# Performance work log

Hardware: AMD Instinct MI355X
Metric: run time of the kernel (lower is better)

The kernel has to match this reference:

```python
import jax, jax.numpy as jnp
import numpy as np

VOCAB_FACTORS = (16, 16, 16, 8)   # prod = 32768 = vocab_size
DIM_FACTORS = (4, 4, 4, 4)        # prod = 256   = projection_dim
RANKS = (1, 16, 16, 16, 1)        # tt_rank = 16
NUM_CORES = 4


def _core_shapes():
    return [(RANKS[k], VOCAB_FACTORS[k], DIM_FACTORS[k], RANKS[k + 1])
            for k in range(NUM_CORES)]


def _vocab_strides():
    # big-endian mixed-radix decomposition of a flat vocab index
    strides = []
    s = 1
    for n in reversed(VOCAB_FACTORS):
        strides.append(s)
        s *= n
    return tuple(reversed(strides))


def tt_lookup(cores, idx):
    """Reconstruct embedding rows from TT cores.
    cores[k]: [r_k, n_k, m_k, r_{k+1}];  idx: int array [...].
    Returns [..., prod(m_k)]."""
    flat = idx.reshape(-1)                                # [Bf]
    res = jnp.ones((flat.shape[0], 1, 1), dtype=cores[0].dtype)  # [Bf, M=1, r=1]
    for core, n, st in zip(cores, VOCAB_FACTORS, _vocab_strides()):
        digit = (flat // st) % n                          # [Bf]
        g = jnp.moveaxis(core[:, digit], 1, 0)            # [Bf, r, m, r']
        res = jnp.einsum('bMr,brms->bMms', res, g)        # [Bf, M, m, r']
        res = res.reshape(res.shape[0], -1, res.shape[-1])  # [Bf, M*m, r']
    D = res.shape[1]
    return res[..., 0].reshape(idx.shape + (D,))


def setup_inputs() -> dict:
    key = jax.random.key(0)
    ks = jax.random.split(key, 12)
    B, NEG, V = 8192, 20, int(np.prod(VOCAB_FACTORS))
    inp = {
        'center_words': jax.random.randint(ks[0], (B, 1), 0, V),
        'target_words': jax.random.randint(ks[1], (B, 1), 0, V),
        'negative_words': jax.random.randint(ks[2], (B, NEG), 0, V),
    }
    # embedding_v: glorot-style init spread over cores
    for k, shp in enumerate(_core_shapes()):
        glorot_std = float(np.sqrt(2.0 / (shp[0] * shp[1] + shp[2] * shp[3])))
        inp[f'v_core{k}'] = glorot_std * jax.random.normal(ks[3 + k], shp, dtype=jnp.float32)
    # embedding_u: stddev=1e-4 per the module
    for k, shp in enumerate(_core_shapes()):
        inp[f'u_core{k}'] = 1e-4 * jax.random.normal(ks[7 + k], shp, dtype=jnp.float32)
    return inp


def reference(center_words, target_words, negative_words,
              v_core0, v_core1, v_core2, v_core3,
              u_core0, u_core1, u_core2, u_core3):
    v_cores = (v_core0, v_core1, v_core2, v_core3)
    u_cores = (u_core0, u_core1, u_core2, u_core3)
    center_embeds = tt_lookup(v_cores, center_words)      # [B, 1, D]
    target_embeds = tt_lookup(u_cores, target_words)      # [B, 1, D]
    neg_embeds = -tt_lookup(u_cores, negative_words)      # [B, K, D]
    # target.bmm(center^T).squeeze(2) -> [B, 1]
    positive_score = jnp.einsum('bsd,btd->bs', target_embeds, center_embeds)
    # sum over negatives then view [B, 1]
    negative_score = jnp.sum(
        jnp.einsum('bkd,btd->bk', neg_embeds, center_embeds),
        axis=1, keepdims=True)                            # [B, 1]
    loss = jax.nn.log_sigmoid(positive_score) + jax.nn.log_sigmoid(negative_score)
    return -jnp.mean(loss)
```

## Files before the change

### kernel.cpp

```cpp
#include <hip/hip_runtime.h>
#include <hip/hip_bf16.h>

#define DEVINL __device__ __forceinline__

constexpr int NNEG   = 20;
constexpr int NBATCH = 8192;
constexpr int NMAIN_BLOCKS = NBATCH / 4;

constexpr int OFF_H01V = 68608;
constexpr int OFF_H23V = 134144;
constexpr int OFF_H01U = 166912;
constexpr int OFF_H23U = 232448;
constexpr int OFF_PART = 265216;
constexpr int OFF_UTAB_F = 267268;
constexpr size_t UTAB4_BYTES = (size_t)32768 * 128;
constexpr size_t USCALE_BYTE_OFF = (size_t)OFF_UTAB_F * 4 + UTAB4_BYTES;
constexpr size_t WS_NEED_BYTES = USCALE_BYTE_OFF + (size_t)32768 * 4;

DEVINL float bfbits_to_f32(unsigned short h) {
  unsigned int u = ((unsigned int)h) << 16;
  float f;
  __builtin_memcpy(&f, &u, sizeof(f));
  return f;
}

DEVINL unsigned short f32_to_bfbits(float f) {
  __hip_bfloat16 h = __float2bfloat16(f);
  unsigned short hb;
  __builtin_memcpy(&hb, &h, 2);
  return hb;
}

DEVINL float ldconv(const void* s, int i, bool isF32) {
  return isF32 ? ((const float*)s)[i]
               : bfbits_to_f32(((const unsigned short*)s)[i]);
}

DEVINL bool sniff_is_f32(const void* probe) {
  const unsigned short* p = (const unsigned short*)probe;
  int insane = 0;
#pragma unroll 1
  for (int i = 0; i < 64; ++i) {
    unsigned short h = p[i];
    int e = (h >> 7) & 0xFF;
    if (h != 0 && (e < 90 || e > 140)) insane++;
  }
  return insane > 8;
}

__global__ __launch_bounds__(256) void tt_htables(
    const void* v0, const void* v1, const void* v2, const void* v3,
    const void* u0, const void* u1, const void* u2, const void* u3,
    float* __restrict__ ws) {
  __shared__ bool sIsF32;
  if (threadIdx.x == 0) sIsF32 = sniff_is_f32(v1);
  __syncthreads();
  const bool isF32 = sIsF32;

  int t = blockIdx.x * 256 + threadIdx.x;
  bool isU = t >= 98304;
  int lt = isU ? t - 98304 : t;
  const void* c0 = isU ? u0 : v0;
  const void* c1 = isU ? u1 : v1;
  const void* c2 = isU ? u2 : v2;
  const void* c3 = isU ? u3 : v3;
  float* dst = ws + (isU ? OFF_H01U : OFF_H01V);

  if (lt < 65536) {
    int combo = lt >> 8, e = lt & 255;
    int d0 = combo >> 4, d1 = combo & 15;
    int M01 = e >> 4, r2 = e & 15;
    int m0 = M01 >> 2, m1 = M01 & 3;
    float s = 0.f;
#pragma unroll
    for (int r1 = 0; r1 < 16; ++r1)
      s = fmaf(ldconv(c0, (d0 * 4 + m0) * 16 + r1, isF32),
               ldconv(c1, ((r1 * 16 + d1) * 4 + m1) * 16 + r2, isF32), s);
    dst[lt] = s;
  } else {
    int lt2 = lt - 65536;
    int combo = lt2 >> 8, e = lt2 & 255;
    int d2 = combo >> 3, d3 = combo & 7;
    int m23 = e >> 4, r2 = e & 15;
    int m2 = m23 >> 2, m3 = m23 & 3;
    float s = 0.f;
#pragma unroll
    for (int r3 = 0; r3 < 16; ++r3)
      s = fmaf(ldconv(c2, ((r2 * 16 + d2) * 4 + m2) * 16 + r3, isF32),
               ldconv(c3, (r3 * 8 + d3) * 4 + m3, isF32), s);
    dst[65536 + lt2] = s;
  }
}

DEVINL float4 ld4(const float* p) { return *reinterpret_cast<const float4*>(p); }

DEVINL float logsigf(float x) {
  return fminf(x, 0.0f) - log1pf(expf(-fabsf(x)));
}

__global__ __launch_bounds__(256) void tt_utab4(const float* __restrict__ ws,
                                                unsigned short* __restrict__ utab4,
                                                float* __restrict__ uscale) {
  const int w    = blockIdx.x * 4 + (threadIdx.x >> 6);
  const int l    = threadIdx.x & 63;
  const int lo   = w & 127;
  const int hi0  = (w >> 7) * 8;

  const float* Bt = ws + OFF_H23U + lo * 256 + (l & 3) * 64;
  float b[64];
#pragma unroll
  for (int i = 0; i < 16; ++i) *reinterpret_cast<float4*>(&b[4 * i]) = ld4(Bt + 4 * i);

  const float* Abase = ws + OFF_H01U + (size_t)hi0 * 256 + (l >> 2) * 16;

#pragma unroll
  for (int rr = 0; rr < 8; rr += 2) {
    float a0[16], a1[16];
#pragma unroll
    for (int i = 0; i < 4; ++i) {
      *reinterpret_cast<float4*>(&a0[4 * i]) = ld4(Abase + rr * 256 + 4 * i);
      *reinterpret_cast<float4*>(&a1[4 * i]) = ld4(Abase + (rr + 1) * 256 + 4 * i);
    }
    float e0[4] = {0.f, 0.f, 0.f, 0.f}, e1[4] = {0.f, 0.f, 0.f, 0.f};
#pragma unroll
    for (int r = 0; r < 16; ++r) {
#pragma unroll
      for (int j = 0; j < 4; ++j) {
        e0[j] = fmaf(a0[r], b[j * 16 + r], e0[j]);
        e1[j] = fmaf(a1[r], b[j * 16 + r], e1[j]);
      }
    }
    float m0 = fmaxf(fmaxf(fabsf(e0[0]), fabsf(e0[1])), fmaxf(fabsf(e0[2]), fabsf(e0[3])));
    float m1 = fmaxf(fmaxf(fabsf(e1[0]), fabsf(e1[1])), fmaxf(fabsf(e1[2]), fabsf(e1[3])));
#pragma unroll
    for (int off = 32; off > 0; off >>= 1) {
      m0 = fmaxf(m0, __shfl_xor(m0, off, 64));
      m1 = fmaxf(m1, __shfl_xor(m1, off, 64));
    }
    const float inv0 = (m0 > 0.f) ? 7.f / m0 : 0.f;
    const float inv1 = (m1 > 0.f) ? 7.f / m1 : 0.f;
    unsigned int p0 = 0, p1 = 0;
#pragma unroll
    for (int j = 0; j < 4; ++j) {
      p0 |= ((unsigned int)(__float2int_rn(e0[j] * inv0) & 15)) << (4 * j);
      p1 |= ((unsigned int)(__float2int_rn(e1[j] * inv1) & 15)) << (4 * j);
    }
    const size_t v0i = (size_t)(hi0 + rr) * 128 + lo;
    const size_t v1i = v0i + 128;
    utab4[v0i * 64 + l] = (unsigned short)p0;
    utab4[v1i * 64 + l] = (unsigned short)p1;
    if (l == 0) {
      uscale[v0i] = m0 * (1.f / 7.f);
      uscale[v1i] = m1 * (1.f / 7.f);
    }
  }
}

__global__ __launch_bounds__(256) void tt_main6(
    const int* __restrict__ cw, const int* __restrict__ tw, const int* __restrict__ nw,
    const float* __restrict__ ws, const unsigned short* __restrict__ utab4,
    const float* __restrict__ uscale, float* __restrict__ partials) {
  const int lane = threadIdx.x & 63;
  const int wid  = threadIdx.x >> 6;
  const int b    = blockIdx.x * 4 + wid;

  const int ci = cw[b];
  const int ti = tw[b];
  const int myneg = nw[b * NNEG + (lane < NNEG ? lane : 0)];

  float c[4] = {0.f, 0.f, 0.f, 0.f};
  {
    const float* A  = ws + OFF_H01V + (ci >> 7) * 256 + (lane >> 2) * 16;
    const float* Bt = ws + OFF_H23V + (ci & 127) * 256 + (lane & 3) * 64;
    float a[16];
#pragma unroll
    for (int i = 0; i < 4; ++i) *reinterpret_cast<float4*>(&a[4 * i]) = ld4(A + 4 * i);
#pragma unroll
    for (int j = 0; j < 4; ++j) {
#pragma unroll
      for (int i = 0; i < 4; ++i) {
        float4 bv = ld4(Bt + j * 16 + 4 * i);
        c[j] = fmaf(a[4 * i], bv.x,
               fmaf(a[4 * i + 1], bv.y,
               fmaf(a[4 * i + 2], bv.z,
               fmaf(a[4 * i + 3], bv.w, c[j]))));
      }
    }
  }

  float pos = 0.f, nacc = 0.f;
#pragma unroll
  for (int k = 0; k < 21; ++k) {
    int idx = (k == 0) ? ti : __shfl(myneg, k - 1, 64);
    idx = __builtin_amdgcn_readfirstlane(idx);
    const unsigned int u = utab4[(size_t)idx * 64 + lane];
    const float sc = uscale[idx];
    const float f0 = (float)(((int)((u)       & 15) ^ 8) - 8);
    const float f1 = (float)(((int)((u >> 4)  & 15) ^ 8) - 8);
    const float f2 = (float)(((int)((u >> 8)  & 15) ^ 8) - 8);
    const float f3 = (float)(((int)((u >> 12) & 15) ^ 8) - 8);
    float p = fmaf(f0, c[0], fmaf(f1, c[1], fmaf(f2, c[2], f3 * c[3]))) * sc;
    if (k == 0) pos = p; else nacc += p;
  }

#pragma unroll
  for (int off = 32; off > 0; off >>= 1) {
    pos  += __shfl_xor(pos, off, 64);
    nacc += __shfl_xor(nacc, off, 64);
  }

  __shared__ float sred[4];
  if (lane == 0) sred[wid] = -(logsigf(pos) + logsigf(-nacc));
  __syncthreads();
  if (threadIdx.x == 0)
    partials[blockIdx.x] = sred[0] + sred[1] + sred[2] + sred[3];
}

DEVINL void frag16(const float* __restrict__ A, const float* __restrict__ Bt,
                   int l, float e[4]) {
  const float* Ar = A + (l >> 2) * 16;
  const float* Br = Bt + (l & 3) * 64;
  float a[16], bb[64];
#pragma unroll
  for (int i = 0; i < 4; ++i) *reinterpret_cast<float4*>(&a[4 * i]) = ld4(Ar + 4 * i);
#pragma unroll
  for (int i = 0; i < 16; ++i) *reinterpret_cast<float4*>(&bb[4 * i]) = ld4(Br + 4 * i);
  e[0] = e[1] = e[2] = e[3] = 0.f;
#pragma unroll
  for (int r = 0; r < 16; ++r) {
#pragma unroll
    for (int j = 0; j < 4; ++j) e[j] = fmaf(a[r], bb[j * 16 + r], e[j]);
  }
}

__global__ __launch_bounds__(256) void tt_sgns_main(
    const int* __restrict__ cw, const int* __restrict__ tw, const int* __restrict__ nw,
    const float* __restrict__ ws, float* __restrict__ partials) {
  const int lane = threadIdx.x & 63;
  const int wid  = threadIdx.x >> 6;
  const int b    = blockIdx.x * 4 + wid;

  const int ci = cw[b];
  const int ti = tw[b];
  const int myneg = nw[b * NNEG + (lane < NNEG ? lane : 0)];

  float c[4];
  frag16(ws + OFF_H01V + (ci >> 7) * 256, ws + OFF_H23V + (ci & 127) * 256, lane, c);

  float pos = 0.f, nacc = 0.f;
#pragma unroll 1
  for (int k = 0; k < 21; ++k) {
    const int idx = (k == 0) ? ti : __shfl(myneg, k - 1, 64);
    float e[4];
    frag16(ws + OFF_H01U + (idx >> 7) * 256, ws + OFF_H23U + (idx & 127) * 256, lane, e);
    float p = fmaf(e[0], c[0], fmaf(e[1], c[1], fmaf(e[2], c[2], e[3] * c[3])));
    if (k == 0) pos = p; else nacc += p;
  }

#pragma unroll
  for (int off = 32; off > 0; off >>= 1) {
    pos  += __shfl_xor(pos, off, 64);
    nacc += __shfl_xor(nacc, off, 64);
  }

  __shared__ float sred[4];
  if (lane == 0) sred[wid] = -(logsigf(pos) + logsigf(-nacc));
  __syncthreads();
  if (threadIdx.x == 0)
    partials[blockIdx.x] = sred[0] + sred[1] + sred[2] + sred[3];
}

__global__ void tt_reduce(const float* __restrict__ partials, void* __restrict__ out) {
  float s = 0.f;
  for (int i = threadIdx.x; i < NMAIN_BLOCKS; i += 256) s += partials[i];
#pragma unroll
  for (int off = 32; off > 0; off >>= 1) s += __shfl_xor(s, off, 64);
  __shared__ float sr[4];
  int lane = threadIdx.x & 63, wid = threadIdx.x >> 6;
  if (lane == 0) sr[wid] = s;
  __syncthreads();
  if (threadIdx.x == 0) {
    float res = (sr[0] + sr[1] + sr[2] + sr[3]) * (1.0f / 8192.0f);
    unsigned short hb = f32_to_bfbits(res);
    unsigned int word = (((unsigned int)hb) << 16) | (unsigned int)hb;
    *(unsigned int*)out = word;
  }
}

extern "C" void kernel_launch(void* const* d_in, const int* in_sizes, int n_in,
                              void* d_out, int out_size, void* d_ws, size_t ws_size,
                              hipStream_t stream) {
  const int* cw = (const int*)d_in[0];
  const int* tw = (const int*)d_in[1];
  const int* nw = (const int*)d_in[2];
  float* ws = (float*)d_ws;

  tt_htables<<<768, 256, 0, stream>>>(
      d_in[3], d_in[4], d_in[5], d_in[6], d_in[7], d_in[8], d_in[9], d_in[10], ws);

  if (ws_size >= WS_NEED_BYTES) {
    unsigned short* utab4 = (unsigned short*)(ws + OFF_UTAB_F);
    float* uscale = (float*)((char*)d_ws + USCALE_BYTE_OFF);
    tt_utab4<<<1024, 256, 0, stream>>>(ws, utab4, uscale);
    tt_main6<<<NMAIN_BLOCKS, 256, 0, stream>>>(
        cw, tw, nw, ws, utab4, uscale, ws + OFF_PART);
  } else {
    tt_sgns_main<<<NMAIN_BLOCKS, 256, 0, stream>>>(cw, tw, nw, ws, ws + OFF_PART);
  }
  tt_reduce<<<1, 256, 0, stream>>>(ws + OFF_PART, d_out);
}
```

Before: 57.41 us.

## Fuse TT table construction into quantized U-table build kernel

Merges the htables kernel and the 4-bit U table kernel into a single tt_build kernel. Each block recomputes the U-side H01 and H23 slices it needs directly into shared memory, with padded rows to avoid bank conflicts. The first 384 blocks also write the V-side tables to global memory. This drops one kernel launch and the global round trip of the U tables, at the cost of redundant recomputation of H01/H23 U rows across blocks.

```diff
diff --git a/kernel.cpp b/kernel.cpp
--- a/kernel.cpp
+++ b/kernel.cpp
@@ -48,78 +48,93 @@
   return insane > 8;
 }
 
-__global__ __launch_bounds__(256) void tt_htables(
+DEVINL float4 ld4(const float* p) { return *reinterpret_cast<const float4*>(p); }
+DEVINL float4 ld4s(const float* p) { return *reinterpret_cast<const float4*>(p); }
+
+DEVINL float logsigf(float x) {
+  return fminf(x, 0.0f) - log1pf(expf(-fabsf(x)));
+}
+
+DEVINL float h01_elem(const void* c0, const void* c1, int combo, int e, bool isF32) {
+  int d0 = combo >> 4, d1 = combo & 15;
+  int M01 = e >> 4, r2 = e & 15;
+  int m0 = M01 >> 2, m1 = M01 & 3;
+  float s = 0.f;
+#pragma unroll
+  for (int r1 = 0; r1 < 16; ++r1)
+    s = fmaf(ldconv(c0, (d0 * 4 + m0) * 16 + r1, isF32),
+             ldconv(c1, ((r1 * 16 + d1) * 4 + m1) * 16 + r2, isF32), s);
+  return s;
+}
+
+DEVINL float h23t_elem(const void* c2, const void* c3, int combo, int e, bool isF32) {
+  int d2 = combo >> 3, d3 = combo & 7;
+  int m23 = e >> 4, r2 = e & 15;
+  int m2 = m23 >> 2, m3 = m23 & 3;
+  float s = 0.f;
+#pragma unroll
+  for (int r3 = 0; r3 < 16; ++r3)
+    s = fmaf(ldconv(c2, ((r2 * 16 + d2) * 4 + m2) * 16 + r3, isF32),
+             ldconv(c3, (r3 * 8 + d3) * 4 + m3, isF32), s);
+  return s;
+}
+
+__global__ __launch_bounds__(256) void tt_build(
     const void* v0, const void* v1, const void* v2, const void* v3,
     const void* u0, const void* u1, const void* u2, const void* u3,
-    float* __restrict__ ws) {
+    float* __restrict__ ws, unsigned short* __restrict__ utab4,
+    float* __restrict__ uscale) {
+  __shared__ float sA[8 * 320];
+  __shared__ float sB[4 * 256];
   __shared__ bool sIsF32;
-  if (threadIdx.x == 0) sIsF32 = sniff_is_f32(v1);
+
+  const int t = threadIdx.x;
+  if (t == 0) sIsF32 = sniff_is_f32(v1);
   __syncthreads();
   const bool isF32 = sIsF32;
 
-  int t = blockIdx.x * 256 + threadIdx.x;
-  bool isU = t >= 98304;
-  int lt = isU ? t - 98304 : t;
-  const void* c0 = isU ? u0 : v0;
-  const void* c1 = isU ? u1 : v1;
-  const void* c2 = isU ? u2 : v2;
-  const void* c3 = isU ? u3 : v3;
-  float* dst = ws + (isU ? OFF_H01U : OFF_H01V);
-
-  if (lt < 65536) {
-    int combo = lt >> 8, e = lt & 255;
-    int d0 = combo >> 4, d1 = combo & 15;
-    int M01 = e >> 4, r2 = e & 15;
-    int m0 = M01 >> 2, m1 = M01 & 3;
-    float s = 0.f;
-#pragma unroll
-    for (int r1 = 0; r1 < 16; ++r1)
-      s = fmaf(ldconv(c0, (d0 * 4 + m0) * 16 + r1, isF32),
-               ldconv(c1, ((r1 * 16 + d1) * 4 + m1) * 16 + r2, isF32), s);
-    dst[lt] = s;
-  } else {
-    int lt2 = lt - 65536;
-    int combo = lt2 >> 8, e = lt2 & 255;
-    int d2 = combo >> 3, d3 = combo & 7;
-    int m23 = e >> 4, r2 = e & 15;
-    int m2 = m23 >> 2, m3 = m23 & 3;
-    float s = 0.f;
-#pragma unroll
-    for (int r3 = 0; r3 < 16; ++r3)
-      s = fmaf(ldconv(c2, ((r2 * 16 + d2) * 4 + m2) * 16 + r3, isF32),
-               ldconv(c3, (r3 * 8 + d3) * 4 + m3, isF32), s);
-    dst[65536 + lt2] = s;
-  }
-}
-
-DEVINL float4 ld4(const float* p) { return *reinterpret_cast<const float4*>(p); }
-
-DEVINL float logsigf(float x) {
-  return fminf(x, 0.0f) - log1pf(expf(-fabsf(x)));
-}
-
-__global__ __launch_bounds__(256) void tt_utab4(const float* __restrict__ ws,
-                                                unsigned short* __restrict__ utab4,
-                                                float* __restrict__ uscale) {
-  const int w    = blockIdx.x * 4 + (threadIdx.x >> 6);
-  const int l    = threadIdx.x & 63;
-  const int lo   = w & 127;
-  const int hi0  = (w >> 7) * 8;
-
-  const float* Bt = ws + OFF_H23U + lo * 256 + (l & 3) * 64;
+  const int lo0 = (blockIdx.x & 31) * 4;
+  const int hi0 = (blockIdx.x >> 5) * 8;
+
+  if (blockIdx.x < 384) {
+    int vt = blockIdx.x * 256 + t;
+    if (vt < 65536) {
+      ws[OFF_H01V + vt] = h01_elem(v0, v1, vt >> 8, vt & 255, isF32);
+    } else {
+      int lt2 = vt - 65536;
+      ws[OFF_H23V + lt2] = h23t_elem(v2, v3, lt2 >> 8, lt2 & 255, isF32);
+    }
+  }
+
+  {
+    const int q = t >> 4, r2 = t & 15;
+#pragma unroll
+    for (int rr = 0; rr < 8; ++rr)
+      sA[rr * 320 + q * 20 + r2] = h01_elem(u0, u1, hi0 + rr, t, isF32);
+#pragma unroll
+    for (int lw = 0; lw < 4; ++lw)
+      sB[lw * 256 + t] = h23t_elem(u2, u3, lo0 + lw, t, isF32);
+  }
+  __syncthreads();
+
+  const int wid = t >> 6;
+  const int l   = t & 63;
+  const int lo  = lo0 + wid;
+
   float b[64];
 #pragma unroll
-  for (int i = 0; i < 16; ++i) *reinterpret_cast<float4*>(&b[4 * i]) = ld4(Bt + 4 * i);
-
-  const float* Abase = ws + OFF_H01U + (size_t)hi0 * 256 + (l >> 2) * 16;
+  for (int i = 0; i < 16; ++i)
+    *reinterpret_cast<float4*>(&b[4 * i]) = ld4s(&sB[wid * 256 + (l & 3) * 64 + 4 * i]);
+
+  const float* Abase = &sA[(l >> 2) * 20];
 
 #pragma unroll
   for (int rr = 0; rr < 8; rr += 2) {
     float a0[16], a1[16];
 #pragma unroll
     for (int i = 0; i < 4; ++i) {
-      *reinterpret_cast<float4*>(&a0[4 * i]) = ld4(Abase + rr * 256 + 4 * i);
-      *reinterpret_cast<float4*>(&a1[4 * i]) = ld4(Abase + (rr + 1) * 256 + 4 * i);
+      *reinterpret_cast<float4*>(&a0[4 * i]) = ld4s(Abase + rr * 320 + 4 * i);
+      *reinterpret_cast<float4*>(&a1[4 * i]) = ld4s(Abase + (rr + 1) * 320 + 4 * i);
     }
     float e0[4] = {0.f, 0.f, 0.f, 0.f}, e1[4] = {0.f, 0.f, 0.f, 0.f};
 #pragma unroll
@@ -216,6 +231,31 @@
     partials[blockIdx.x] = sred[0] + sred[1] + sred[2] + sred[3];
 }
 
+__global__ __launch_bounds__(256) void tt_htables(
+    const void* v0, const void* v1, const void* v2, const void* v3,
+    const void* u0, const void* u1, const void* u2, const void* u3,
+    float* __restrict__ ws) {
+  __shared__ bool sIsF32;
+  if (threadIdx.x == 0) sIsF32 = sniff_is_f32(v1);
+  __syncthreads();
+  const bool isF32 = sIsF32;
+
+  int t = blockIdx.x * 256 + threadIdx.x;
+  bool isU = t >= 98304;
+  int lt = isU ? t - 98304 : t;
+  const void* c0 = isU ? u0 : v0;
+  const void* c1 = isU ? u1 : v1;
+  const void* c2 = isU ? u2 : v2;
+  const void* c3 = isU ? u3 : v3;
+  float* dst = ws + (isU ? OFF_H01U : OFF_H01V);
+
+  if (lt < 65536) dst[lt] = h01_elem(c0, c1, lt >> 8, lt & 255, isF32);
+  else {
+    int lt2 = lt - 65536;
+    dst[65536 + lt2] = h23t_elem(c2, c3, lt2 >> 8, lt2 & 255, isF32);
+  }
+}
+
 DEVINL void frag16(const float* __restrict__ A, const float* __restrict__ Bt,
                    int l, float e[4]) {
   const float* Ar = A + (l >> 2) * 16;
@@ -295,16 +335,17 @@
   const int* nw = (const int*)d_in[2];
   float* ws = (float*)d_ws;
 
-  tt_htables<<<768, 256, 0, stream>>>(
-      d_in[3], d_in[4], d_in[5], d_in[6], d_in[7], d_in[8], d_in[9], d_in[10], ws);
-
   if (ws_size >= WS_NEED_BYTES) {
     unsigned short* utab4 = (unsigned short*)(ws + OFF_UTAB_F);
     float* uscale = (float*)((char*)d_ws + USCALE_BYTE_OFF);
-    tt_utab4<<<1024, 256, 0, stream>>>(ws, utab4, uscale);
+    tt_build<<<1024, 256, 0, stream>>>(
+        d_in[3], d_in[4], d_in[5], d_in[6], d_in[7], d_in[8], d_in[9], d_in[10],
+        ws, utab4, uscale);
     tt_main6<<<NMAIN_BLOCKS, 256, 0, stream>>>(
         cw, tw, nw, ws, utab4, uscale, ws + OFF_PART);
   } else {
+    tt_htables<<<768, 256, 0, stream>>>(
+        d_in[3], d_in[4], d_in[5], d_in[6], d_in[7], d_in[8], d_in[9], d_in[10], ws);
     tt_sgns_main<<<NMAIN_BLOCKS, 256, 0, stream>>>(cw, tw, nw, ws, ws + OFF_PART);
   }
   tt_reduce<<<1, 256, 0, stream>>>(ws + OFF_PART, d_out);
```

Result: slower. 82.03 us (+42.9%).
